# Optimization experiments

Hardware: AMD Instinct MI355X
Metric: run time of the kernel (lower is better)

Reference implementation:

```python
import jax, jax.numpy as jnp
import numpy as np

N_SRC, N_DST, N_EDGES, E = 100000, 50000, 600000, 128

def setup_inputs() -> dict:
    key = jax.random.key(0)
    k1, k2, k3, k4, k5, k6 = jax.random.split(key, 6)
    return {
        "h_src": jax.random.normal(k1, (N_SRC, E), dtype=jnp.float32),
        "weights": jax.random.uniform(k2, (N_EDGES,), dtype=jnp.float32),
        "src_idx": jax.random.randint(k3, (N_EDGES,), 0, N_SRC, dtype=jnp.int32),
        "dst_idx": jax.random.randint(k4, (N_EDGES,), 0, N_DST, dtype=jnp.int32),
        "num_dst": N_DST,
        "q_w": jax.random.normal(k5, (E, E), dtype=jnp.float32) * (2.0 / np.sqrt(E + E)),  # xavier-ish, gain=sqrt(2)
        "q_b": jnp.zeros((E,), dtype=jnp.float32),
        "w_w": jax.random.normal(k6, (E, 2 * E), dtype=jnp.float32) * (2.0 / np.sqrt(E + 2 * E)),
        "w_b": jnp.zeros((E,), dtype=jnp.float32),
    }

def reference(h_src, weights, src_idx, dst_idx, num_dst, q_w, q_b, w_w, w_b):
    h_dst = h_src[:num_dst]                                  # [n_dst, E]
    n = jax.nn.relu(h_src @ q_w.T + q_b)                     # [n_src, E] (dropout=eval/no-op)
    w = weights.astype(jnp.float32)
    m = n[src_idx] * w[:, None]                              # [n_edges, E] edge messages
    agg = jax.ops.segment_sum(m, dst_idx, num_segments=num_dst)   # weighted feature sum
    ws = jax.ops.segment_sum(w, dst_idx, num_segments=num_dst)    # weight sum
    ws = jnp.clip(ws, 1.0, None)[:, None]                    # clamp(min=1)
    z = jnp.concatenate([h_dst, agg / ws], axis=1)           # [n_dst, 2E]
    z = jax.nn.relu(z @ w_w.T + w_b)                         # [n_dst, E]
    z_norm = jnp.linalg.norm(z, axis=1, keepdims=True)
    z_norm = jnp.where(z_norm == 0, 1.0, z_norm)
    return z / z_norm
```

## Files before the change

### kernel.cpp

```cpp
#include <hip/hip_runtime.h>
#include <math.h>


typedef __attribute__((ext_vector_type(8))) short  short8;
typedef __attribute__((ext_vector_type(8))) __bf16 bf16x8;
typedef __attribute__((ext_vector_type(4))) float  f32x4;

#define MFMA16(a, b, c) __builtin_amdgcn_mfma_f32_16x16x32_bf16( \
    __builtin_bit_cast(bf16x8, (a)), __builtin_bit_cast(bf16x8, (b)), (c), 0, 0, 0)

#define EDGE_CAP 2048

__device__ __forceinline__ ushort f2bf(float x) {
    unsigned u = __float_as_uint(x);
    return (ushort)((u + 0x7fffu + ((u >> 16) & 1u)) >> 16);
}
__device__ __forceinline__ float bfhi(unsigned p) { return __uint_as_float(p & 0xffff0000u); }
__device__ __forceinline__ float bflo(unsigned p) { return __uint_as_float(p << 16); }

__device__ __forceinline__ short8 cvt8(float4 v0, float4 v1) {
    ushort t[8] = { f2bf(v0.x), f2bf(v0.y), f2bf(v0.z), f2bf(v0.w),
                    f2bf(v1.x), f2bf(v1.y), f2bf(v1.z), f2bf(v1.w) };
    return *(short8*)t;
}

__global__ __launch_bounds__(512) void k_gemm1_hist(const float* __restrict__ h,
    const float* __restrict__ qw, const float* __restrict__ qb,
    ushort* __restrict__ nout, int nrows, int t1,
    const int* __restrict__ dst, int* __restrict__ hist, int nedges, int nb)
{
    __shared__ __align__(16) ushort aL[128 * 128];
    __shared__ __align__(16) ushort bL[128 * 128];
    const int tid = threadIdx.x;

    if (blockIdx.x >= t1) {
        int* hl = (int*)aL;
        const int g = blockIdx.x - t1;
        const int G = gridDim.x - t1;
        for (int i = tid; i < nb; i += 512) hl[i] = 0;
        __syncthreads();
        const int chunk = (nedges + G - 1) / G;
        const int e0 = g * chunk, e1 = min(e0 + chunk, nedges);
        for (int e = e0 + tid; e < e1; e += 512)
            atomicAdd(&hl[dst[e] >> 5], 1);
        __syncthreads();
        for (int i = tid; i < nb; i += 512) hist[i * G + g] = hl[i];
        return;
    }

    const int rb = blockIdx.x * 128;
    const int rr = tid >> 4, sl = tid & 15;

    #pragma unroll
    for (int rg = 0; rg < 4; ++rg) {
        int row = rg * 32 + rr, gr = rb + row;
        float4 a0 = make_float4(0.f,0.f,0.f,0.f), a1 = a0;
        if (gr < nrows) {
            a0 = *(const float4*)&h[(size_t)gr * 128 + sl * 8];
            a1 = *(const float4*)&h[(size_t)gr * 128 + sl * 8 + 4];
        }
        *(short8*)&aL[row * 128 + (sl ^ (row & 7)) * 8] = cvt8(a0, a1);
        float4 b0 = *(const float4*)&qw[row * 128 + sl * 8];
        float4 b1 = *(const float4*)&qw[row * 128 + sl * 8 + 4];
        *(short8*)&bL[row * 128 + (sl ^ (row & 7)) * 8] = cvt8(b0, b1);
    }
    __syncthreads();

    const int w = tid >> 6, l = tid & 63;
    const int lr = l & 15, lk = l >> 4;
    const int row = w * 16 + lr;

    short8 a[4];
    #pragma unroll
    for (int ks = 0; ks < 4; ++ks)
        a[ks] = *(const short8*)&aL[row * 128 + ((ks * 4 + lk) ^ (lr & 7)) * 8];

    f32x4 acc[8];
    #pragma unroll
    for (int nt = 0; nt < 8; ++nt) acc[nt] = (f32x4){0.f, 0.f, 0.f, 0.f};

    #pragma unroll
    for (int nt = 0; nt < 8; ++nt)
        #pragma unroll
        for (int ks = 0; ks < 4; ++ks) {
            short8 b = *(const short8*)&bL[(nt * 16 + lr) * 128 + ((ks * 4 + lk) ^ (lr & 7)) * 8];
            acc[nt] = MFMA16(b, a[ks], acc[nt]);
        }

    const int gr = rb + row;
    if (gr < nrows) {
        #pragma unroll
        for (int nt = 0; nt < 8; ++nt) {
            float4 bv = *(const float4*)&qb[nt * 16 + lk * 4];
            ushort t[4];
            t[0] = f2bf(fmaxf(acc[nt][0] + bv.x, 0.f));
            t[1] = f2bf(fmaxf(acc[nt][1] + bv.y, 0.f));
            t[2] = f2bf(fmaxf(acc[nt][2] + bv.z, 0.f));
            t[3] = f2bf(fmaxf(acc[nt][3] + bv.w, 0.f));
            *(ushort4*)&nout[(size_t)gr * 128 + nt * 16 + lk * 4] = *(ushort4*)t;
        }
    }
}

__global__ __launch_bounds__(1024) void k_scan_blk(const int* __restrict__ counts,
    int* __restrict__ offs, int* __restrict__ partials, int n)
{
    __shared__ int wtot[16];
    const int tid = threadIdx.x, lane = tid & 63, wv = tid >> 6;
    const int idx = blockIdx.x * 1024 + tid;
    int v = (idx < n) ? counts[idx] : 0;
    int x = v;
    #pragma unroll
    for (int off = 1; off < 64; off <<= 1) {
        int y = __shfl_up(x, off);
        if (lane >= off) x += y;
    }
    if (lane == 63) wtot[wv] = x;
    __syncthreads();
    if (tid == 0) {
        int r = 0;
        #pragma unroll
        for (int q = 0; q < 16; ++q) { int t = wtot[q]; wtot[q] = r; r += t; }
    }
    __syncthreads();
    if (idx < n) offs[idx] = wtot[wv] + x - v;
    if (tid == 1023) partials[blockIdx.x] = wtot[15] + x;
}

__global__ void k_scan_part(int* __restrict__ partials, int nb)
{
    __shared__ int wsum4[4];
    const int tid = threadIdx.x, lane = tid & 63, wv = tid >> 6;
    int v = (tid < nb) ? partials[tid] : 0;
    int x = v;
    #pragma unroll
    for (int off = 1; off < 64; off <<= 1) {
        int y = __shfl_up(x, off);
        if (lane >= off) x += y;
    }
    if (lane == 63) wsum4[wv] = x;
    __syncthreads();
    if (tid == 0) {
        int r = 0;
        #pragma unroll
        for (int q = 0; q < 4; ++q) { int t = wsum4[q]; wsum4[q] = r; r += t; }
    }
    __syncthreads();
    if (tid < nb) partials[tid] = wsum4[wv] + x - v;
}

__global__ __launch_bounds__(256) void k_part(const int* __restrict__ src,
    const int* __restrict__ dst, const float* __restrict__ w,
    const int* __restrict__ binoff0, const int* __restrict__ parts,
    int2* __restrict__ eb, int nedges, int nb)
{
    __shared__ int cur[2048];
    const int g = blockIdx.x, tid = threadIdx.x, G = gridDim.x;
    for (int b = tid; b < nb; b += 256) {
        int i = b * G + g;
        cur[b] = binoff0[i] + parts[i >> 10];
    }
    __syncthreads();
    const int chunk = (nedges + G - 1) / G;
    const int e0 = g * chunk, e1 = min(e0 + chunk, nedges);
    for (int e = e0 + tid; e < e1; e += 256) {
        int d = dst[e];
        int pos = atomicAdd(&cur[d >> 5], 1);
        eb[pos] = make_int2(((d & 31) << 17) | src[e], __float_as_int(w[e]));
    }
}

__global__ __launch_bounds__(256) void k_bsort_gather(const ushort* __restrict__ nsrc,
    const int2* __restrict__ eb, const int* __restrict__ binoff0,
    const int* __restrict__ parts, ushort* __restrict__ z2,
    int ndst, int nedges, int G, int NB)
{
    __shared__ int2 els[EDGE_CAP];
    __shared__ int  base[33];
    __shared__ int  cur[32];
    const int b = blockIdx.x, tid = threadIdx.x;
    const int i0 = b * G;
    const int j0 = binoff0[i0] + parts[i0 >> 10];
    int j1 = nedges;
    if (b != NB - 1) {
        int i1 = (b + 1) * G;
        j1 = binoff0[i1] + parts[i1 >> 10];
    }
    const int cnt_e = j1 - j0;

    if (tid < 32) cur[tid] = 0;
    __syncthreads();
    for (int j = j0 + tid; j < j1; j += 256)
        atomicAdd(&cur[eb[j].x >> 17], 1);
    __syncthreads();

    if (tid < 64) {
        int a = (tid < 32) ? cur[tid] : 0;
        int x = a;
        #pragma unroll
        for (int off = 1; off < 64; off <<= 1) {
            int y = __shfl_up(x, off);
            if (tid >= off) x += y;
        }
        if (tid < 32) {
            base[tid] = x - a;
            cur[tid]  = x - a;
        }
        if (tid == 31) base[32] = x;
    }
    __syncthreads();

    const int wv = tid >> 6, lane = tid & 63;
    const int g = lane >> 4, s = lane & 15;

    if (cnt_e <= EDGE_CAP) {
        for (int j = j0 + tid; j < j1; j += 256) {
            int2 e = eb[j];
            int pos = atomicAdd(&cur[e.x >> 17], 1);
            els[pos] = make_int2(e.x & 0x1FFFF, e.y);
        }
        __syncthreads();

        for (int r = wv; r < 32; r += 4) {
            int gr = b * 32 + r;
            if (gr >= ndst) break;
            const int ja = j0 + base[r], jb = j0 + base[r + 1];
            float acc[8] = {0.f,0.f,0.f,0.f,0.f,0.f,0.f,0.f};
            float ws = 0.f;
            for (int j = ja + g; j < jb; j += 4) {
                int2 ew = els[j - j0];
                float we = __int_as_float(ew.y);
                short8 rv = *(const short8*)&nsrc[(size_t)ew.x * 128 + s * 8];
                uint4 p = __builtin_bit_cast(uint4, rv);
                acc[0] = fmaf(bflo(p.x), we, acc[0]);
                acc[1] = fmaf(bfhi(p.x), we, acc[1]);
                acc[2] = fmaf(bflo(p.y), we, acc[2]);
                acc[3] = fmaf(bfhi(p.y), we, acc[3]);
                acc[4] = fmaf(bflo(p.z), we, acc[4]);
                acc[5] = fmaf(bfhi(p.z), we, acc[5]);
                acc[6] = fmaf(bflo(p.w), we, acc[6]);
                acc[7] = fmaf(bfhi(p.w), we, acc[7]);
                ws += we;
            }
            #pragma unroll
            for (int i = 0; i < 8; ++i) {
                acc[i] += __shfl_xor(acc[i], 16);
                acc[i] += __shfl_xor(acc[i], 32);
            }
            ws += __shfl_xor(ws, 16);
            ws += __shfl_xor(ws, 32);
            if (g == 0) {
                float inv = 1.f / fmaxf(ws, 1.f);
                ushort t8[8];
                #pragma unroll
                for (int i = 0; i < 8; ++i) t8[i] = f2bf(acc[i] * inv);
                *(short8*)&z2[(size_t)gr * 128 + s * 8] = *(short8*)t8;
            }
        }
    } else {
        for (int r = wv; r < 32; r += 4) {
            int gr = b * 32 + r;
            if (gr >= ndst) break;
            float acc[8] = {0.f,0.f,0.f,0.f,0.f,0.f,0.f,0.f};
            float ws = 0.f;
            for (int j = j0 + g; j < j1; j += 4) {
                int2 e = eb[j];
                if ((e.x >> 17) != r) continue;
                float we = __int_as_float(e.y);
                short8 rv = *(const short8*)&nsrc[(size_t)(e.x & 0x1FFFF) * 128 + s * 8];
                uint4 p = __builtin_bit_cast(uint4, rv);
                acc[0] = fmaf(bflo(p.x), we, acc[0]);
                acc[1] = fmaf(bfhi(p.x), we, acc[1]);
                acc[2] = fmaf(bflo(p.y), we, acc[2]);
                acc[3] = fmaf(bfhi(p.y), we, acc[3]);
                acc[4] = fmaf(bflo(p.z), we, acc[4]);
                acc[5] = fmaf(bfhi(p.z), we, acc[5]);
                acc[6] = fmaf(bflo(p.w), we, acc[6]);
                acc[7] = fmaf(bfhi(p.w), we, acc[7]);
                ws += we;
            }
            #pragma unroll
            for (int i = 0; i < 8; ++i) {
                acc[i] += __shfl_xor(acc[i], 16);
                acc[i] += __shfl_xor(acc[i], 32);
            }
            ws += __shfl_xor(ws, 16);
            ws += __shfl_xor(ws, 32);
            if (g == 0) {
                float inv = 1.f / fmaxf(ws, 1.f);
                ushort t8[8];
                #pragma unroll
                for (int i = 0; i < 8; ++i) t8[i] = f2bf(acc[i] * inv);
                *(short8*)&z2[(size_t)gr * 128 + s * 8] = *(short8*)t8;
            }
        }
    }
}

__global__ __launch_bounds__(512) void k_gemm2(const float* __restrict__ h,
    const ushort* __restrict__ z2, const float* __restrict__ ww,
    const float* __restrict__ wb, float* __restrict__ out, int nrows)
{
    __shared__ __align__(16) ushort aL[128 * 128];
    __shared__ __align__(16) ushort bL[128 * 128];
    const int tid = threadIdx.x;
    const int rb  = blockIdx.x * 128;
    const int rr = tid >> 4, sl = tid & 15;

    const int w = tid >> 6, l = tid & 63;
    const int lr = l & 15, lk = l >> 4;
    const int row = w * 16 + lr;

    f32x4 acc[8];
    #pragma unroll
    for (int nt = 0; nt < 8; ++nt) acc[nt] = (f32x4){0.f, 0.f, 0.f, 0.f};

    #pragma unroll
    for (int ph = 0; ph < 2; ++ph) {
        if (ph) __syncthreads();
        #pragma unroll
        for (int rg = 0; rg < 4; ++rg) {
            int r2 = rg * 32 + rr, gr = rb + r2;
            short8 av = (short8){0,0,0,0,0,0,0,0};
            if (gr < nrows) {
                if (ph == 0) {
                    float4 a0 = *(const float4*)&h[(size_t)gr * 128 + sl * 8];
                    float4 a1 = *(const float4*)&h[(size_t)gr * 128 + sl * 8 + 4];
                    av = cvt8(a0, a1);
                } else {
                    av = *(const short8*)&z2[(size_t)gr * 128 + sl * 8];
                }
            }
            *(short8*)&aL[r2 * 128 + (sl ^ (r2 & 7)) * 8] = av;
            float4 b0 = *(const float4*)&ww[r2 * 256 + ph * 128 + sl * 8];
            float4 b1 = *(const float4*)&ww[r2 * 256 + ph * 128 + sl * 8 + 4];
            *(short8*)&bL[r2 * 128 + (sl ^ (r2 & 7)) * 8] = cvt8(b0, b1);
        }
        __syncthreads();

        short8 a[4];
        #pragma unroll
        for (int ks = 0; ks < 4; ++ks)
            a[ks] = *(const short8*)&aL[row * 128 + ((ks * 4 + lk) ^ (lr & 7)) * 8];

        #pragma unroll
        for (int nt = 0; nt < 8; ++nt)
            #pragma unroll
            for (int ks = 0; ks < 4; ++ks) {
                short8 b = *(const short8*)&bL[(nt * 16 + lr) * 128 + ((ks * 4 + lk) ^ (lr & 7)) * 8];
                acc[nt] = MFMA16(b, a[ks], acc[nt]);
            }
    }

    float val[8][4];
    float ss = 0.f;
    #pragma unroll
    for (int nt = 0; nt < 8; ++nt) {
        float4 bv = *(const float4*)&wb[nt * 16 + lk * 4];
        #pragma unroll
        for (int v = 0; v < 4; ++v) {
            float x = acc[nt][v] + ((const float*)&bv)[v];
            x = fmaxf(x, 0.f);
            val[nt][v] = x;
            ss = fmaf(x, x, ss);
        }
    }
    ss += __shfl_xor(ss, 16);
    ss += __shfl_xor(ss, 32);
    float nr = sqrtf(ss);
    nr = (nr == 0.f) ? 1.f : nr;
    float inv = 1.f / nr;

    const int gr = rb + row;
    if (gr < nrows) {
        #pragma unroll
        for (int nt = 0; nt < 8; ++nt) {
            float4 o;
            o.x = val[nt][0] * inv; o.y = val[nt][1] * inv;
            o.z = val[nt][2] * inv; o.w = val[nt][3] * inv;
            *(float4*)&out[(size_t)gr * 128 + nt * 16 + lk * 4] = o;
        }
    }
}

extern "C" void kernel_launch(void* const* d_in, const int* in_sizes, int n_in,
                              void* d_out, int out_size, void* d_ws, size_t ws_size,
                              hipStream_t stream)
{
    const float* h   = (const float*)d_in[0];
    const float* wts = (const float*)d_in[1];
    const int*   src = (const int*)d_in[2];
    const int*   dst = (const int*)d_in[3];
    const float* qw  = (const float*)d_in[5];
    const float* qb  = (const float*)d_in[6];
    const float* www = (const float*)d_in[7];
    const float* wb  = (const float*)d_in[8];
    float* out = (float*)d_out;

    const int n_src   = in_sizes[0] / 128;
    const int n_edges = in_sizes[1];
    const int n_dst   = out_size / 128;

    const int G  = 128;
    const int NB = (n_dst + 31) / 32;
    const int NBINS = NB * G;

    ushort* nbuf    = (ushort*)d_ws;
    ushort* z2      = nbuf + (size_t)n_src * 128;
    int2*   eb      = (int2*)(z2 + (size_t)n_dst * 128);
    int*    hist    = (int*)(eb + n_edges);
    int*    binoff0 = hist + NBINS;
    int*    parts   = binoff0 + NBINS;

    const int t1 = (n_src + 127) / 128;
    k_gemm1_hist<<<t1 + G, 512, 0, stream>>>(h, qw, qb, nbuf, n_src, t1,
                                             dst, hist, n_edges, NB);

    const int nbs = (NBINS + 1023) / 1024;
    k_scan_blk<<<nbs, 1024, 0, stream>>>(hist, binoff0, parts, NBINS);
    k_scan_part<<<1, 256, 0, stream>>>(parts, nbs);

    k_part<<<G, 256, 0, stream>>>(src, dst, wts, binoff0, parts, eb, n_edges, NB);

    k_bsort_gather<<<NB, 256, 0, stream>>>(nbuf, eb, binoff0, parts, z2,
                                           n_dst, n_edges, G, NB);

    const int t2 = (n_dst + 127) / 128;
    k_gemm2<<<t2, 512, 0, stream>>>(h, z2, www, wb, out, n_dst);
}
```

Before: 95.11 us.

## Overlap edge partitioning with gemm1, fold partial scan into consumers, unroll gather

The histogram becomes its own kernel, so the edge partition pass can run in the same launch as the first GEMM rather than the histogram. The separate single-block partial-sum scan kernel is removed; each consumer block rescans the small partials array in shared memory, which cuts one launch at the cost of some redundant work. The gather loop now processes two edges per iteration, issuing two independent row loads to raise memory-level parallelism, with a predicated second edge.

```diff
diff --git a/kernel.cpp b/kernel.cpp
--- a/kernel.cpp
+++ b/kernel.cpp
@@ -24,31 +24,99 @@
     return *(short8*)t;
 }
 
-__global__ __launch_bounds__(512) void k_gemm1_hist(const float* __restrict__ h,
-    const float* __restrict__ qw, const float* __restrict__ qb,
-    ushort* __restrict__ nout, int nrows, int t1,
-    const int* __restrict__ dst, int* __restrict__ hist, int nedges, int nb)
+__global__ __launch_bounds__(512) void k_hist(const int* __restrict__ dst,
+    int* __restrict__ hist, int nedges, int nb)
+{
+    __shared__ int hl[2048];
+    const int g = blockIdx.x, tid = threadIdx.x, G = gridDim.x;
+    for (int i = tid; i < nb; i += 512) hl[i] = 0;
+    __syncthreads();
+    const int chunk = (nedges + G - 1) / G;
+    const int e0 = g * chunk, e1 = min(e0 + chunk, nedges);
+    for (int e = e0 + tid; e < e1; e += 512)
+        atomicAdd(&hl[dst[e] >> 5], 1);
+    __syncthreads();
+    for (int i = tid; i < nb; i += 512) hist[i * G + g] = hl[i];
+}
+
+__global__ __launch_bounds__(1024) void k_scan_blk(const int* __restrict__ counts,
+    int* __restrict__ offs, int* __restrict__ partials, int n)
+{
+    __shared__ int wtot[16];
+    const int tid = threadIdx.x, lane = tid & 63, wv = tid >> 6;
+    const int idx = blockIdx.x * 1024 + tid;
+    int v = (idx < n) ? counts[idx] : 0;
+    int x = v;
+    #pragma unroll
+    for (int off = 1; off < 64; off <<= 1) {
+        int y = __shfl_up(x, off);
+        if (lane >= off) x += y;
+    }
+    if (lane == 63) wtot[wv] = x;
+    __syncthreads();
+    if (tid == 0) {
+        int r = 0;
+        #pragma unroll
+        for (int q = 0; q < 16; ++q) { int t = wtot[q]; wtot[q] = r; r += t; }
+    }
+    __syncthreads();
+    if (idx < n) offs[idx] = wtot[wv] + x - v;
+    if (tid == 1023) partials[blockIdx.x] = wtot[15] + x;
+}
+
+__global__ __launch_bounds__(512) void k_part_gemm1(
+    const int* __restrict__ src, const int* __restrict__ dst,
+    const float* __restrict__ w, const int* __restrict__ binoff0,
+    const int* __restrict__ partials, int2* __restrict__ eb,
+    int nedges, int nb, int nbs, int G,
+    const float* __restrict__ h, const float* __restrict__ qw,
+    const float* __restrict__ qb, ushort* __restrict__ nout, int nrows)
 {
     __shared__ __align__(16) ushort aL[128 * 128];
     __shared__ __align__(16) ushort bL[128 * 128];
+    __shared__ int wtmp[8];
     const int tid = threadIdx.x;
 
-    if (blockIdx.x >= t1) {
-        int* hl = (int*)aL;
-        const int g = blockIdx.x - t1;
-        const int G = gridDim.x - t1;
-        for (int i = tid; i < nb; i += 512) hl[i] = 0;
+    if (blockIdx.x < G) {
+        int* cur   = (int*)aL;
+        int* pscan = (int*)bL;
+        const int g = blockIdx.x;
+        {
+            const int lane = tid & 63, wv = tid >> 6;
+            int v = (tid < nbs) ? partials[tid] : 0;
+            int x = v;
+            #pragma unroll
+            for (int off = 1; off < 64; off <<= 1) {
+                int y = __shfl_up(x, off);
+                if (lane >= off) x += y;
+            }
+            if (lane == 63) wtmp[wv] = x;
+            __syncthreads();
+            if (tid == 0) {
+                int r = 0;
+                #pragma unroll
+                for (int q = 0; q < 4; ++q) { int t = wtmp[q]; wtmp[q] = r; r += t; }
+            }
+            __syncthreads();
+            if (tid < nbs) pscan[tid] = wtmp[wv] + x - v;
+        }
+        __syncthreads();
+        for (int b = tid; b < nb; b += 512) {
+            int i = b * G + g;
+            cur[b] = binoff0[i] + pscan[i >> 10];
+        }
         __syncthreads();
         const int chunk = (nedges + G - 1) / G;
         const int e0 = g * chunk, e1 = min(e0 + chunk, nedges);
-        for (int e = e0 + tid; e < e1; e += 512)
-            atomicAdd(&hl[dst[e] >> 5], 1);
-        __syncthreads();
-        for (int i = tid; i < nb; i += 512) hist[i * G + g] = hl[i];
+        for (int e = e0 + tid; e < e1; e += 512) {
+            int d = dst[e];
+            int pos = atomicAdd(&cur[d >> 5], 1);
+            eb[pos] = make_int2(((d & 31) << 17) | src[e], __float_as_int(w[e]));
+        }
         return;
     }
 
-    const int rb = blockIdx.x * 128;
+    const int rb = (blockIdx.x - G) * 128;
     const int rr = tid >> 4, sl = tid & 15;
 
     #pragma unroll
@@ -66,9 +134,9 @@
     }
     __syncthreads();
 
-    const int w = tid >> 6, l = tid & 63;
+    const int w_ = tid >> 6, l = tid & 63;
     const int lr = l & 15, lk = l >> 4;
-    const int row = w * 16 + lr;
+    const int row = w_ * 16 + lr;
 
     short8 a[4];
     #pragma unroll
@@ -102,94 +170,49 @@
     }
 }
 
-__global__ __launch_bounds__(1024) void k_scan_blk(const int* __restrict__ counts,
-    int* __restrict__ offs, int* __restrict__ partials, int n)
-{
-    __shared__ int wtot[16];
-    const int tid = threadIdx.x, lane = tid & 63, wv = tid >> 6;
-    const int idx = blockIdx.x * 1024 + tid;
-    int v = (idx < n) ? counts[idx] : 0;
-    int x = v;
-    #pragma unroll
-    for (int off = 1; off < 64; off <<= 1) {
-        int y = __shfl_up(x, off);
-        if (lane >= off) x += y;
-    }
-    if (lane == 63) wtot[wv] = x;
-    __syncthreads();
-    if (tid == 0) {
-        int r = 0;
-        #pragma unroll
-        for (int q = 0; q < 16; ++q) { int t = wtot[q]; wtot[q] = r; r += t; }
-    }
-    __syncthreads();
-    if (idx < n) offs[idx] = wtot[wv] + x - v;
-    if (tid == 1023) partials[blockIdx.x] = wtot[15] + x;
-}
-
-__global__ void k_scan_part(int* __restrict__ partials, int nb)
-{
-    __shared__ int wsum4[4];
-    const int tid = threadIdx.x, lane = tid & 63, wv = tid >> 6;
-    int v = (tid < nb) ? partials[tid] : 0;
-    int x = v;
-    #pragma unroll
-    for (int off = 1; off < 64; off <<= 1) {
-        int y = __shfl_up(x, off);
-        if (lane >= off) x += y;
-    }
-    if (lane == 63) wsum4[wv] = x;
-    __syncthreads();
-    if (tid == 0) {
-        int r = 0;
-        #pragma unroll
-        for (int q = 0; q < 4; ++q) { int t = wsum4[q]; wsum4[q] = r; r += t; }
-    }
-    __syncthreads();
-    if (tid < nb) partials[tid] = wsum4[wv] + x - v;
-}
-
-__global__ __launch_bounds__(256) void k_part(const int* __restrict__ src,
-    const int* __restrict__ dst, const float* __restrict__ w,
-    const int* __restrict__ binoff0, const int* __restrict__ parts,
-    int2* __restrict__ eb, int nedges, int nb)
-{
-    __shared__ int cur[2048];
-    const int g = blockIdx.x, tid = threadIdx.x, G = gridDim.x;
-    for (int b = tid; b < nb; b += 256) {
-        int i = b * G + g;
-        cur[b] = binoff0[i] + parts[i >> 10];
-    }
-    __syncthreads();
-    const int chunk = (nedges + G - 1) / G;
-    const int e0 = g * chunk, e1 = min(e0 + chunk, nedges);
-    for (int e = e0 + tid; e < e1; e += 256) {
-        int d = dst[e];
-        int pos = atomicAdd(&cur[d >> 5], 1);
-        eb[pos] = make_int2(((d & 31) << 17) | src[e], __float_as_int(w[e]));
-    }
-}
-
 __global__ __launch_bounds__(256) void k_bsort_gather(const ushort* __restrict__ nsrc,
     const int2* __restrict__ eb, const int* __restrict__ binoff0,
-    const int* __restrict__ parts, ushort* __restrict__ z2,
-    int ndst, int nedges, int G, int NB)
+    const int* __restrict__ partials, ushort* __restrict__ z2,
+    int ndst, int nedges, int G, int NB, int nbs)
 {
     __shared__ int2 els[EDGE_CAP];
+    __shared__ int  pscan[256];
     __shared__ int  base[33];
     __shared__ int  cur[32];
+    __shared__ int  wtmp[4];
     const int b = blockIdx.x, tid = threadIdx.x;
+
+    {
+        const int lane = tid & 63, wv = tid >> 6;
+        int v = (tid < nbs) ? partials[tid] : 0;
+        int x = v;
+        #pragma unroll
+        for (int off = 1; off < 64; off <<= 1) {
+            int y = __shfl_up(x, off);
+            if (lane >= off) x += y;
+        }
+        if (lane == 63) wtmp[wv] = x;
+        __syncthreads();
+        if (tid == 0) {
+            int r = 0;
+            #pragma unroll
+            for (int q = 0; q < 4; ++q) { int t = wtmp[q]; wtmp[q] = r; r += t; }
+        }
+        __syncthreads();
+        if (tid < nbs) pscan[tid] = wtmp[wv] + x - v;
+    }
+    if (tid < 32) cur[tid] = 0;
+    __syncthreads();
+
     const int i0 = b * G;
-    const int j0 = binoff0[i0] + parts[i0 >> 10];
+    const int j0 = binoff0[i0] + pscan[i0 >> 10];
     int j1 = nedges;
     if (b != NB - 1) {
         int i1 = (b + 1) * G;
-        j1 = binoff0[i1] + parts[i1 >> 10];
+        j1 = binoff0[i1] + pscan[i1 >> 10];
     }
     const int cnt_e = j1 - j0;
 
-    if (tid < 32) cur[tid] = 0;
-    __syncthreads();
     for (int j = j0 + tid; j < j1; j += 256)
         atomicAdd(&cur[eb[j].x >> 17], 1);
     __syncthreads();
@@ -224,23 +247,36 @@
         for (int r = wv; r < 32; r += 4) {
             int gr = b * 32 + r;
             if (gr >= ndst) break;
-            const int ja = j0 + base[r], jb = j0 + base[r + 1];
+            const int ja = base[r], jb = base[r + 1];
             float acc[8] = {0.f,0.f,0.f,0.f,0.f,0.f,0.f,0.f};
             float ws = 0.f;
-            for (int j = ja + g; j < jb; j += 4) {
-                int2 ew = els[j - j0];
-                float we = __int_as_float(ew.y);
-                short8 rv = *(const short8*)&nsrc[(size_t)ew.x * 128 + s * 8];
-                uint4 p = __builtin_bit_cast(uint4, rv);
-                acc[0] = fmaf(bflo(p.x), we, acc[0]);
-                acc[1] = fmaf(bfhi(p.x), we, acc[1]);
-                acc[2] = fmaf(bflo(p.y), we, acc[2]);
-                acc[3] = fmaf(bfhi(p.y), we, acc[3]);
-                acc[4] = fmaf(bflo(p.z), we, acc[4]);
-                acc[5] = fmaf(bfhi(p.z), we, acc[5]);
-                acc[6] = fmaf(bflo(p.w), we, acc[6]);
-                acc[7] = fmaf(bfhi(p.w), we, acc[7]);
-                ws += we;
+            for (int j = ja + g; j < jb; j += 8) {
+                int2 e1 = els[j];
+                bool has2 = (j + 4 < jb);
+                int2 e2 = has2 ? els[j + 4] : e1;
+                float w1 = __int_as_float(e1.y);
+                float w2 = has2 ? __int_as_float(e2.y) : 0.f;
+                short8 r1 = *(const short8*)&nsrc[(size_t)e1.x * 128 + s * 8];
+                short8 r2 = *(const short8*)&nsrc[(size_t)e2.x * 128 + s * 8];
+                uint4 p1 = __builtin_bit_cast(uint4, r1);
+                uint4 p2 = __builtin_bit_cast(uint4, r2);
+                acc[0] = fmaf(bflo(p1.x), w1, acc[0]);
+                acc[1] = fmaf(bfhi(p1.x), w1, acc[1]);
+                acc[2] = fmaf(bflo(p1.y), w1, acc[2]);
+                acc[3] = fmaf(bfhi(p1.y), w1, acc[3]);
+                acc[4] = fmaf(bflo(p1.z), w1, acc[4]);
+                acc[5] = fmaf(bfhi(p1.z), w1, acc[5]);
+                acc[6] = fmaf(bflo(p1.w), w1, acc[6]);
+                acc[7] = fmaf(bfhi(p1.w), w1, acc[7]);
+                acc[0] = fmaf(bflo(p2.x), w2, acc[0]);
+                acc[1] = fmaf(bfhi(p2.x), w2, acc[1]);
+                acc[2] = fmaf(bflo(p2.y), w2, acc[2]);
+                acc[3] = fmaf(bfhi(p2.y), w2, acc[3]);
+                acc[4] = fmaf(bflo(p2.z), w2, acc[4]);
+                acc[5] = fmaf(bfhi(p2.z), w2, acc[5]);
+                acc[6] = fmaf(bflo(p2.w), w2, acc[6]);
+                acc[7] = fmaf(bfhi(p2.w), w2, acc[7]);
+                ws += w1 + w2;
             }
             #pragma unroll
             for (int i = 0; i < 8; ++i) {
@@ -404,6 +440,7 @@
     const int G  = 128;
     const int NB = (n_dst + 31) / 32;
     const int NBINS = NB * G;
+    const int nbs = (NBINS + 1023) / 1024;
 
     ushort* nbuf    = (ushort*)d_ws;
     ushort* z2      = nbuf + (size_t)n_src * 128;
@@ -412,18 +449,17 @@
     int*    binoff0 = hist + NBINS;
     int*    parts   = binoff0 + NBINS;
 
+    k_hist<<<G, 512, 0, stream>>>(dst, hist, n_edges, NB);
+
+    k_scan_blk<<<nbs, 1024, 0, stream>>>(hist, binoff0, parts, NBINS);
+
     const int t1 = (n_src + 127) / 128;
-    k_gemm1_hist<<<t1 + G, 512, 0, stream>>>(h, qw, qb, nbuf, n_src, t1,
-                                             dst, hist, n_edges, NB);
-
-    const int nbs = (NBINS + 1023) / 1024;
-    k_scan_blk<<<nbs, 1024, 0, stream>>>(hist, binoff0, parts, NBINS);
-    k_scan_part<<<1, 256, 0, stream>>>(parts, nbs);
-
-    k_part<<<G, 256, 0, stream>>>(src, dst, wts, binoff0, parts, eb, n_edges, NB);
+    k_part_gemm1<<<G + t1, 512, 0, stream>>>(src, dst, wts, binoff0, parts, eb,
+                                             n_edges, NB, nbs, G,
+                                             h, qw, qb, nbuf, n_src);
 
     k_bsort_gather<<<NB, 256, 0, stream>>>(nbuf, eb, binoff0, parts, z2,
-                                           n_dst, n_edges, G, NB);
+                                           n_dst, n_edges, G, NB, nbs);
 
     const int t2 = (n_dst + 127) / 128;
     k_gemm2<<<t2, 512, 0, stream>>>(h, z2, www, wb, out, n_dst);
```

Measured after the change: 86.56 us. 1.1x faster.
